# Kernel tuning notes

Measured on AMD Instinct MI355X. Metric: run time of the kernel, lower is better.

## Reference

```python
import jax, jax.numpy as jnp
import numpy as np

D_MODEL = 256

def setup_inputs() -> dict:
    key = jax.random.key(0)
    k1, k2, k3, k4, k5, k6 = jax.random.split(key, 6)
    B, LQ, LK, D = 16, 2048, 2048, D_MODEL
    q = jax.random.normal(k1, (B, LQ, D), dtype=jnp.float32)
    k = jax.random.normal(k2, (B, LK, D), dtype=jnp.float32)
    tsp = jax.random.normal(k3, (B, LK, D), dtype=jnp.float32)
    # xavier_uniform for w_qk [D, D] (no bias)
    bound = float(np.sqrt(6.0 / (D + D)))
    w_qk = jax.random.uniform(k4, (D, D), minval=-bound, maxval=bound, dtype=jnp.float32)
    # linear1: default torch init kaiming-uniform-ish; any values fine for correctness baseline
    lim = float(1.0 / np.sqrt(D))
    w1 = jax.random.uniform(k5, (D, D), minval=-lim, maxval=lim, dtype=jnp.float32)
    b1 = jax.random.uniform(k6, (D,), minval=-lim, maxval=lim, dtype=jnp.float32)
    return {"q": q, "k": k, "tsp": tsp, "w_qk": w_qk, "w1": w1, "b1": b1}

def reference(q, k, tsp, w_qk, w1, b1):
    d_head = q.shape[-1]
    temperature = jnp.asarray(np.power(d_head, 0.5), dtype=q.dtype)
    residual = q
    # shared Q/K projection (torch Linear: x @ W^T)
    qp = jnp.einsum('bqd,ed->bqe', q, w_qk)            # [B, Lq, Dh]
    kp = jnp.einsum('bkd,ed->bke', k, w_qk)            # [B, Lk, Dh]
    logits = jnp.einsum('bqd,bkd->bqk', qp, kp) / temperature  # [B, Lq, Lk]
    attn = jax.nn.softmax(logits, axis=2)
    # sigmoid is monotonic: max(sigmoid(x)) == sigmoid(max(x))
    prob_fg = jax.nn.sigmoid(jnp.max(logits, axis=-1, keepdims=True))  # [B, Lq, 1]
    out = jnp.einsum('bqk,bkd->bqd', attn, tsp)        # [B, Lq, Dh]
    gated = (residual + out) * prob_fg
    return jnp.einsum('bqd,ed->bqe', gated, w1) + b1
```

## Files before the change

kernel.cpp:

```cpp
#include <hip/hip_runtime.h>
#include <hip/hip_bf16.h>

typedef __bf16 bf16;
typedef __bf16 bf16x8 __attribute__((ext_vector_type(8)));
typedef __bf16 bf16x4 __attribute__((ext_vector_type(4)));
typedef float f32x4 __attribute__((ext_vector_type(4)));

static __device__ __forceinline__ f32x4 mfma16(bf16x8 a, bf16x8 b, f32x4 c) {
    return __builtin_amdgcn_mfma_f32_16x16x32_bf16(a, b, c, 0, 0, 0);
}

static __device__ __forceinline__ void load16_to_lds(const void* g, void* l) {
    __builtin_amdgcn_global_load_lds(
        (const __attribute__((address_space(1))) unsigned int*)g,
        (__attribute__((address_space(3))) unsigned int*)l, 16, 0, 0);
}

#define LKV 2048
#define DM 256

__global__ void convert_two(const float* __restrict__ a, bf16* __restrict__ da,
                            const float* __restrict__ b, bf16* __restrict__ db) {
    int blk = blockIdx.x;
    const float* src = (blk < 64) ? a : b;
    bf16* dst = (blk < 64) ? da : db;
    int i = (blk & 63) * 256 + threadIdx.x;
    float4 v = *(const float4*)(src + (size_t)i * 4);
    bf16x4 o;
    o[0] = (bf16)v.x; o[1] = (bf16)v.y; o[2] = (bf16)v.z; o[3] = (bf16)v.w;
    *(bf16x4*)(dst + (size_t)i * 4) = o;
}

__global__ __launch_bounds__(256) void transpose_tsp(const float* __restrict__ src,
                                                     bf16* __restrict__ dst) {
    __shared__ float tile[64][65];
    const int tid = threadIdx.x;
    const int b = blockIdx.z;
    const int kv0 = blockIdx.x * 64, d0 = blockIdx.y * 64;
#pragma unroll
    for (int i = 0; i < 4; ++i) {
        int idx = i * 256 + tid;
        int kv = idx >> 4, c4 = (idx & 15) * 4;
        float4 v = *(const float4*)(src + ((long)(b * LKV + kv0 + kv)) * DM + d0 + c4);
        tile[kv][c4 + 0] = v.x; tile[kv][c4 + 1] = v.y;
        tile[kv][c4 + 2] = v.z; tile[kv][c4 + 3] = v.w;
    }
    __syncthreads();
#pragma unroll
    for (int i = 0; i < 2; ++i) {
        int idx = i * 256 + tid;
        int d = idx >> 3, kc = idx & 7;
        bf16x8 o;
#pragma unroll
        for (int j = 0; j < 8; ++j) o[j] = (bf16)tile[kc * 8 + j][d];
        *(bf16x8*)(dst + ((long)(b * DM + d0 + d)) * LKV + kv0 + kc * 8) = o;
    }
}

template<bool IN_BF16, bool OUT_BF16, bool HAS_BIAS>
static __device__ __forceinline__ void gemm_body(const void* __restrict__ Xv,
                                                 const bf16* __restrict__ W,
                                                 const float* __restrict__ bias,
                                                 float scale, void* __restrict__ Y,
                                                 long rowbase) {
    __shared__ __align__(16) bf16 Xl[64][264];
    __shared__ __align__(16) bf16 Wl[256][40];
    const int tid  = threadIdx.x;
    const int lane = tid & 63, wave = tid >> 6;
    const int hi = lane >> 4, lo = lane & 15;

    if (IN_BF16) {
        const bf16* Xb = (const bf16*)Xv;
#pragma unroll
        for (int i = 0; i < 8; ++i) {
            int idx = i * 256 + tid;
            int r = idx >> 5, c8 = (idx & 31) * 8;
            uint4 v = *(const uint4*)(Xb + (rowbase + r) * 256 + c8);
            *(uint4*)(&Xl[r][c8]) = v;
        }
    } else {
        const float* X = (const float*)Xv;
#pragma unroll
        for (int i = 0; i < 16; ++i) {
            int idx4 = i * 256 + tid;
            int e = idx4 * 4;
            int r = e >> 8, c = e & 255;
            float4 v = *(const float4*)(X + (rowbase + r) * 256 + c);
            bf16x4 o;
            o[0] = (bf16)v.x; o[1] = (bf16)v.y; o[2] = (bf16)v.z; o[3] = (bf16)v.w;
            *(bf16x4*)(&Xl[r][c]) = o;
        }
    }

    f32x4 acc[16];
    const f32x4 zero = {0.f, 0.f, 0.f, 0.f};
#pragma unroll
    for (int n = 0; n < 16; ++n) acc[n] = zero;

    for (int ks = 0; ks < 8; ++ks) {
        __syncthreads();
#pragma unroll
        for (int c = 0; c < 4; ++c) {
            int idx = c * 256 + tid;
            int e = idx >> 2, part = idx & 3;
            uint4 v = *(const uint4*)((const char*)W + (size_t)e * 512 + ks * 64 + part * 16);
            *(uint4*)((char*)&Wl[0][0] + e * 80 + part * 16) = v;
        }
        __syncthreads();
        bf16x8 a = *(const bf16x8*)((const char*)&Xl[0][0] + (wave * 16 + lo) * 528 + ks * 64 + hi * 16);
#pragma unroll
        for (int n = 0; n < 16; ++n) {
            bf16x8 bfr = *(const bf16x8*)((const char*)&Wl[0][0] + (n * 16 + lo) * 80 + hi * 16);
            acc[n] = mfma16(a, bfr, acc[n]);
        }
    }

#pragma unroll
    for (int n = 0; n < 16; ++n) {
        int col = n * 16 + lo;
        float bv = HAS_BIAS ? bias[col] : 0.f;
#pragma unroll
        for (int r = 0; r < 4; ++r) {
            long row = rowbase + wave * 16 + hi * 4 + r;
            float v = acc[n][r] * scale + bv;
            if (OUT_BF16) ((bf16*)Y)[row * 256 + col] = (bf16)v;
            else          ((float*)Y)[row * 256 + col] = v;
        }
    }
}

__global__ __launch_bounds__(256) void gemm_qk(const float* __restrict__ q,
                                               const float* __restrict__ k,
                                               const bf16* __restrict__ W,
                                               bf16* __restrict__ qp,
                                               bf16* __restrict__ kp) {
    bool is_k = blockIdx.x >= 512;
    const float* X = is_k ? k : q;
    bf16* Y = is_k ? kp : qp;
    float scale = is_k ? 1.0f : 0.0625f;
    long rowbase = (long)(blockIdx.x & 511) * 64;
    gemm_body<false, true, false>(X, W, nullptr, scale, Y, rowbase);
}

__global__ __launch_bounds__(256) void gemm_out(const bf16* __restrict__ gated,
                                                const bf16* __restrict__ W,
                                                const float* __restrict__ bias,
                                                float* __restrict__ out) {
    gemm_body<true, false, true>(gated, W, bias, 1.0f, out, (long)blockIdx.x * 64);
}

__global__ __launch_bounds__(256, 2) void flash3(const bf16* __restrict__ qp,
                                                 const bf16* __restrict__ kp,
                                                 const bf16* __restrict__ tspT,
                                                 const float* __restrict__ qorig,
                                                 bf16* __restrict__ gated) {
    __shared__ __align__(16) char kp_lds[2][32 * 512];
    __shared__ __align__(16) char tsp_lds[2][256 * 64];
    __shared__ __align__(16) char p_lds[4][16 * 80];
    const int tid  = threadIdx.x;
    const int lane = tid & 63, wave = tid >> 6;
    const int hi = lane >> 4, lo = lane & 15;

    int id  = (int)blockIdx.x;
    int bid = (id & 7) * 64 + (id >> 3);
    const int b  = bid >> 5;
    const int qb = bid & 31;
    const long qbase = (long)b * LKV + qb * 64;
    const char* kp_g  = (const char*)(kp + (long)b * LKV * DM);
    const char* tsp_g = (const char*)(tspT + (long)b * DM * LKV);

    int kp_off[4], tsp_off[4];
#pragma unroll
    for (int j = 0; j < 4; ++j) {
        int kv = wave * 8 + j * 2 + (lane >> 5);
        kp_off[j] = kv * 512 + (((lane & 31) ^ (kv & 7)) << 4);
        int d = wave * 64 + j * 16 + (lane >> 2);
        int cp = (lane & 3) ^ ((lane >> 3) & 3);
        tsp_off[j] = d * 4096 + cp * 16;
    }

    bf16x8 aq[8];
    {
        const bf16* qrow = qp + (qbase + wave * 16 + lo) * DM;
#pragma unroll
        for (int ks = 0; ks < 8; ++ks) aq[ks] = *(const bf16x8*)(qrow + ks * 32 + hi * 8);
    }

    bf16x8 ones;
#pragma unroll
    for (int j = 0; j < 8; ++j) ones[j] = (bf16)1.0f;

    f32x4 o[16], o_l;
    const f32x4 zero = {0.f, 0.f, 0.f, 0.f};
#pragma unroll
    for (int n = 0; n < 16; ++n) o[n] = zero;
    o_l = zero;
    float m[4], tm[4];
#pragma unroll
    for (int r = 0; r < 4; ++r) { m[r] = -1e30f; tm[r] = -1e30f; }

    const int kswz = (lo & 7) << 4;
    const int tswz = ((lo >> 1) & 3) << 4;

#pragma unroll
    for (int j = 0; j < 4; ++j) {
        load16_to_lds(kp_g + kp_off[j],  &kp_lds[0][wave * 4096 + j * 1024]);
        load16_to_lds(tsp_g + tsp_off[j], &tsp_lds[0][wave * 4096 + j * 1024]);
    }
    __syncthreads();

    for (int t = 0; t < 64; ++t) {
        const int cur = t & 1;
        if (t < 63) {
            const long ko = (long)(t + 1);
#pragma unroll
            for (int j = 0; j < 4; ++j) {
                load16_to_lds(kp_g + ko * 16384 + kp_off[j],  &kp_lds[cur ^ 1][wave * 4096 + j * 1024]);
                load16_to_lds(tsp_g + ko * 64 + tsp_off[j],   &tsp_lds[cur ^ 1][wave * 4096 + j * 1024]);
            }
        }

        f32x4 s[2];
        __builtin_amdgcn_s_setprio(1);
#pragma unroll
        for (int n = 0; n < 2; ++n) {
            s[n] = zero;
            const char* rowp = &kp_lds[cur][(n * 16 + lo) << 9];
#pragma unroll
            for (int ks = 0; ks < 8; ++ks) {
                bf16x8 bk = *(const bf16x8*)(rowp + ((ks * 64 + hi * 16) ^ kswz));
                s[n] = mfma16(aq[ks], bk, s[n]);
            }
        }
        __builtin_amdgcn_s_setprio(0);

        float pm[4];
#pragma unroll
        for (int r = 0; r < 4; ++r) {
            float v = fmaxf(s[0][r], s[1][r]);
            v = fmaxf(v, __shfl_xor(v, 1));
            v = fmaxf(v, __shfl_xor(v, 2));
            v = fmaxf(v, __shfl_xor(v, 4));
            v = fmaxf(v, __shfl_xor(v, 8));
            pm[r] = v;
            tm[r] = fmaxf(tm[r], v);
        }
        bool grow = false;
#pragma unroll
        for (int r = 0; r < 4; ++r) grow |= (pm[r] > m[r] + 8.f);
        if (__any(grow)) {
#pragma unroll
            for (int r = 0; r < 4; ++r) {
                float nm = fmaxf(m[r], pm[r]);
                float a = __expf(m[r] - nm);
                m[r] = nm;
                o_l[r] *= a;
#pragma unroll
                for (int n = 0; n < 16; ++n) o[n][r] *= a;
            }
        }

        char* pw = &p_lds[wave][0];
#pragma unroll
        for (int n = 0; n < 2; ++n)
#pragma unroll
            for (int r = 0; r < 4; ++r) {
                float p = __expf(s[n][r] - m[r]);
                *(bf16*)(pw + (hi * 4 + r) * 80 + (n * 16 + lo) * 2) = (bf16)p;
            }

        bf16x8 pa = *(const bf16x8*)(pw + lo * 80 + hi * 16);
        o_l = mfma16(pa, ones, o_l);
        __builtin_amdgcn_s_setprio(1);
#pragma unroll
        for (int dt = 0; dt < 16; ++dt) {
            int d = dt * 16 + lo;
            bf16x8 bt = *(const bf16x8*)(&tsp_lds[cur][d * 64 + ((hi * 16) ^ tswz)]);
            o[dt] = mfma16(pa, bt, o[dt]);
        }
        __builtin_amdgcn_s_setprio(0);

        __syncthreads();
    }

#pragma unroll
    for (int r = 0; r < 4; ++r) {
        float prob = 1.f / (1.f + __expf(-tm[r]));
        float invl = 1.f / o_l[r];
        long row = qbase + wave * 16 + hi * 4 + r;
#pragma unroll
        for (int dt = 0; dt < 16; ++dt) {
            int col = dt * 16 + lo;
            float g = (qorig[row * 256 + col] + o[dt][r] * invl) * prob;
            gated[row * 256 + col] = (bf16)g;
        }
    }
}

extern "C" void kernel_launch(void* const* d_in, const int* in_sizes, int n_in,
                              void* d_out, int out_size, void* d_ws, size_t ws_size,
                              hipStream_t stream) {
    const float* q    = (const float*)d_in[0];
    const float* k    = (const float*)d_in[1];
    const float* tsp  = (const float*)d_in[2];
    const float* w_qk = (const float*)d_in[3];
    const float* w1   = (const float*)d_in[4];
    const float* b1   = (const float*)d_in[5];
    float* out = (float*)d_out;
    char* ws = (char*)d_ws;

    bf16* qp_b  = (bf16*)(ws + 0);
    bf16* kp_b  = (bf16*)(ws + 16777216);
    bf16* tspT  = (bf16*)(ws + 33554432);
    bf16* gated = (bf16*)(ws + 50331648);
    bf16* wqkb  = (bf16*)(ws + 67108864);
    bf16* w1b   = (bf16*)(ws + 67239936);

    convert_two<<<128, 256, 0, stream>>>(w_qk, wqkb, w1, w1b);

    dim3 tg(32, 4, 16);
    transpose_tsp<<<tg, 256, 0, stream>>>(tsp, tspT);

    gemm_qk<<<1024, 256, 0, stream>>>(q, k, wqkb, qp_b, kp_b);

    flash3<<<512, 256, 0, stream>>>(qp_b, kp_b, tspT, q, gated);

    gemm_out<<<512, 256, 0, stream>>>(gated, w1b, b1, out);
}
```

Before: 197.6 us.

## Transpose MFMA operands in flash kernel so P stays in registers via bpermute

Swaps the MFMA operand order so each lane holds a query row's scores transposed (rows along lanes). The online-softmax max then needs only two cross-lane shuffles and one scalar m per lane instead of four. P is repacked into the B-operand layout with ds_bpermute instead of a round trip through per-wave LDS. The epilogue now writes gated with vectorized float4 reads and bf16x4 stores. This removes LDS P traffic and reduction shuffles, at the cost of the bpermute operations and selects.

```diff
diff --git a/kernel.cpp b/kernel.cpp
--- a/kernel.cpp
+++ b/kernel.cpp
@@ -4,6 +4,7 @@
 typedef __bf16 bf16;
 typedef __bf16 bf16x8 __attribute__((ext_vector_type(8)));
 typedef __bf16 bf16x4 __attribute__((ext_vector_type(4)));
+typedef __bf16 bf16x2 __attribute__((ext_vector_type(2)));
 typedef float f32x4 __attribute__((ext_vector_type(4)));
 
 static __device__ __forceinline__ f32x4 mfma16(bf16x8 a, bf16x8 b, f32x4 c) {
@@ -149,14 +150,13 @@
     gemm_body<true, false, true>(gated, W, bias, 1.0f, out, (long)blockIdx.x * 64);
 }
 
-__global__ __launch_bounds__(256, 2) void flash3(const bf16* __restrict__ qp,
+__global__ __launch_bounds__(256, 2) void flash4(const bf16* __restrict__ qp,
                                                  const bf16* __restrict__ kp,
                                                  const bf16* __restrict__ tspT,
                                                  const float* __restrict__ qorig,
                                                  bf16* __restrict__ gated) {
     __shared__ __align__(16) char kp_lds[2][32 * 512];
     __shared__ __align__(16) char tsp_lds[2][256 * 64];
-    __shared__ __align__(16) char p_lds[4][16 * 80];
     const int tid  = threadIdx.x;
     const int lane = tid & 63, wave = tid >> 6;
     const int hi = lane >> 4, lo = lane & 15;
@@ -179,6 +179,11 @@
         tsp_off[j] = d * 4096 + cp * 16;
     }
 
+    int bp_src[4];
+#pragma unroll
+    for (int k2 = 0; k2 < 4; ++k2)
+        bp_src[k2] = ((((hi & 1) * 2 + (k2 >> 1)) << 4) + lo) << 2;
+
     bf16x8 aq[8];
     {
         const bf16* qrow = qp + (qbase + wave * 16 + lo) * DM;
@@ -195,9 +200,7 @@
 #pragma unroll
     for (int n = 0; n < 16; ++n) o[n] = zero;
     o_l = zero;
-    float m[4], tm[4];
-#pragma unroll
-    for (int r = 0; r < 4; ++r) { m[r] = -1e30f; tm[r] = -1e30f; }
+    float m = -1e30f, tm = -1e30f;
 
     const int kswz = (lo & 7) << 4;
     const int tswz = ((lo >> 1) & 3) << 4;
@@ -228,72 +231,72 @@
             const char* rowp = &kp_lds[cur][(n * 16 + lo) << 9];
 #pragma unroll
             for (int ks = 0; ks < 8; ++ks) {
-                bf16x8 bk = *(const bf16x8*)(rowp + ((ks * 64 + hi * 16) ^ kswz));
-                s[n] = mfma16(aq[ks], bk, s[n]);
+                bf16x8 kk = *(const bf16x8*)(rowp + ((ks * 64 + hi * 16) ^ kswz));
+                s[n] = mfma16(kk, aq[ks], s[n]);
             }
         }
         __builtin_amdgcn_s_setprio(0);
 
-        float pm[4];
-#pragma unroll
-        for (int r = 0; r < 4; ++r) {
-            float v = fmaxf(s[0][r], s[1][r]);
-            v = fmaxf(v, __shfl_xor(v, 1));
-            v = fmaxf(v, __shfl_xor(v, 2));
-            v = fmaxf(v, __shfl_xor(v, 4));
-            v = fmaxf(v, __shfl_xor(v, 8));
-            pm[r] = v;
-            tm[r] = fmaxf(tm[r], v);
-        }
-        bool grow = false;
-#pragma unroll
-        for (int r = 0; r < 4; ++r) grow |= (pm[r] > m[r] + 8.f);
-        if (__any(grow)) {
-#pragma unroll
-            for (int r = 0; r < 4; ++r) {
-                float nm = fmaxf(m[r], pm[r]);
-                float a = __expf(m[r] - nm);
-                m[r] = nm;
-                o_l[r] *= a;
-#pragma unroll
-                for (int n = 0; n < 16; ++n) o[n][r] *= a;
+        float pm = fmaxf(fmaxf(fmaxf(s[0][0], s[0][1]), fmaxf(s[0][2], s[0][3])),
+                         fmaxf(fmaxf(s[1][0], s[1][1]), fmaxf(s[1][2], s[1][3])));
+        pm = fmaxf(pm, __shfl_xor(pm, 16));
+        pm = fmaxf(pm, __shfl_xor(pm, 32));
+        tm = fmaxf(tm, pm);
+        if (__any(pm > m + 8.f)) {
+            float nm = fmaxf(m, pm);
+            float a = __expf(m - nm);
+            m = nm;
+            o_l *= a;
+#pragma unroll
+            for (int n = 0; n < 16; ++n) o[n] *= a;
+        }
+
+        int cvt[2][2];
+#pragma unroll
+        for (int n = 0; n < 2; ++n)
+#pragma unroll
+            for (int c = 0; c < 2; ++c) {
+                bf16x2 pr;
+                pr[0] = (bf16)__expf(s[n][2 * c]     - m);
+                pr[1] = (bf16)__expf(s[n][2 * c + 1] - m);
+                cvt[n][c] = __builtin_bit_cast(int, pr);
             }
-        }
-
-        char* pw = &p_lds[wave][0];
-#pragma unroll
-        for (int n = 0; n < 2; ++n)
-#pragma unroll
-            for (int r = 0; r < 4; ++r) {
-                float p = __expf(s[n][r] - m[r]);
-                *(bf16*)(pw + (hi * 4 + r) * 80 + (n * 16 + lo) * 2) = (bf16)p;
-            }
-
-        bf16x8 pa = *(const bf16x8*)(pw + lo * 80 + hi * 16);
-        o_l = mfma16(pa, ones, o_l);
+        int pki[4];
+#pragma unroll
+        for (int k2 = 0; k2 < 4; ++k2) {
+            int a0 = __builtin_amdgcn_ds_bpermute(bp_src[k2], cvt[0][k2 & 1]);
+            int a1 = __builtin_amdgcn_ds_bpermute(bp_src[k2], cvt[1][k2 & 1]);
+            pki[k2] = (hi < 2) ? a0 : a1;
+        }
+        int4 pii = make_int4(pki[0], pki[1], pki[2], pki[3]);
+        bf16x8 pk = __builtin_bit_cast(bf16x8, pii);
+
+        o_l = mfma16(ones, pk, o_l);
         __builtin_amdgcn_s_setprio(1);
 #pragma unroll
         for (int dt = 0; dt < 16; ++dt) {
             int d = dt * 16 + lo;
-            bf16x8 bt = *(const bf16x8*)(&tsp_lds[cur][d * 64 + ((hi * 16) ^ tswz)]);
-            o[dt] = mfma16(pa, bt, o[dt]);
+            bf16x8 tt = *(const bf16x8*)(&tsp_lds[cur][d * 64 + ((hi * 16) ^ tswz)]);
+            o[dt] = mfma16(tt, pk, o[dt]);
         }
         __builtin_amdgcn_s_setprio(0);
 
         __syncthreads();
     }
 
-#pragma unroll
-    for (int r = 0; r < 4; ++r) {
-        float prob = 1.f / (1.f + __expf(-tm[r]));
-        float invl = 1.f / o_l[r];
-        long row = qbase + wave * 16 + hi * 4 + r;
-#pragma unroll
-        for (int dt = 0; dt < 16; ++dt) {
-            int col = dt * 16 + lo;
-            float g = (qorig[row * 256 + col] + o[dt][r] * invl) * prob;
-            gated[row * 256 + col] = (bf16)g;
-        }
+    float prob = 1.f / (1.f + __expf(-tm));
+    float invl = 1.f / o_l[0];
+    long row = qbase + wave * 16 + lo;
+#pragma unroll
+    for (int dt = 0; dt < 16; ++dt) {
+        int c0 = dt * 16 + hi * 4;
+        float4 qv = *(const float4*)(qorig + row * 256 + c0);
+        bf16x4 g;
+        g[0] = (bf16)((qv.x + o[dt][0] * invl) * prob);
+        g[1] = (bf16)((qv.y + o[dt][1] * invl) * prob);
+        g[2] = (bf16)((qv.z + o[dt][2] * invl) * prob);
+        g[3] = (bf16)((qv.w + o[dt][3] * invl) * prob);
+        *(bf16x4*)(gated + row * 256 + c0) = g;
     }
 }
 
@@ -323,7 +326,7 @@
 
     gemm_qk<<<1024, 256, 0, stream>>>(q, k, wqkb, qp_b, kp_b);
 
-    flash3<<<512, 256, 0, stream>>>(qp_b, kp_b, tspT, q, gated);
+    flash4<<<512, 256, 0, stream>>>(qp_b, kp_b, tspT, q, gated);
 
     gemm_out<<<512, 256, 0, stream>>>(gated, w1b, b1, out);
 }
```

New measurement: 182.9 us. 1.08x faster.
